# Performance work log

Hardware: AMD Instinct MI355X
Metric: run time of the kernel (lower is better)

## Reference

```python
import jax, jax.numpy as jnp
import numpy as np

ANCHORS = jnp.array([[1.3221, 1.73145], [3.19275, 4.00944], [5.05587, 8.09892],
                     [9.47112, 4.84053], [11.2364, 10.0071]], dtype=jnp.float32)
NUM_ANCHORS = 5
NUM_CLASSES = 20
MAX_BOXES = 50
NOOBJECT_SCALE = 1.0
OBJECT_SCALE = 5.0
COORD_SCALE = 1.0
CLASS_SCALE = 1.0
SIL_THRESH = 0.6


def iou_cwh(b1, b2):
    # boxes as (cx, cy, w, h); matches repo bbox_ious(x1y1x2y2=False)
    x1, y1, w1, h1 = b1[..., 0], b1[..., 1], b1[..., 2], b1[..., 3]
    x2, y2, w2, h2 = b2[..., 0], b2[..., 1], b2[..., 2], b2[..., 3]
    uw = jnp.maximum(x1 + w1 * 0.5, x2 + w2 * 0.5) - jnp.minimum(x1 - w1 * 0.5, x2 - w2 * 0.5)
    uh = jnp.maximum(y1 + h1 * 0.5, y2 + h2 * 0.5) - jnp.minimum(y1 - h1 * 0.5, y2 - h2 * 0.5)
    cw = w1 + w2 - uw
    ch = h1 + h2 - uh
    inter = jnp.where((cw <= 0) | (ch <= 0), 0.0, cw * ch)
    return inter / (w1 * h1 + w2 * h2 - inter)


def setup_inputs() -> dict:
    key = jax.random.key(0)
    k1, k2, k3, k4 = jax.random.split(key, 4)
    nB = 64
    output = jax.random.normal(k1, (nB, NUM_ANCHORS * (5 + NUM_CLASSES), 38, 38), dtype=jnp.float32)
    # target layout per box: (class, x, y, w, h), all normalized; x>0 marks a valid box
    cls_col = jax.random.randint(k2, (nB, MAX_BOXES, 1), 0, NUM_CLASSES).astype(jnp.float32)
    xy = jax.random.uniform(k3, (nB, MAX_BOXES, 2), minval=0.05, maxval=0.95)
    wh = jax.random.uniform(k4, (nB, MAX_BOXES, 2), minval=0.02, maxval=0.3)
    target = jnp.concatenate([cls_col, xy, wh], axis=-1).reshape(nB, MAX_BOXES * 5)
    return {"output": output, "target": target}


def region_loss(output, target):
    nB = output.shape[0]
    nA, nC = NUM_ANCHORS, NUM_CLASSES
    nH, nW = output.shape[2], output.shape[3]
    out = output.reshape(nB, nA, 5 + nC, nH, nW)
    x = jax.nn.sigmoid(out[:, :, 0])
    y = jax.nn.sigmoid(out[:, :, 1])
    w = out[:, :, 2]
    h = out[:, :, 3]
    conf = jax.nn.sigmoid(out[:, :, 4])
    # [nB,nA,nC,nH,nW] -> [nB*nA*nH*nW, nC] (matches torch transpose/view order)
    cls_logits = jnp.transpose(out[:, :, 5:], (0, 1, 3, 4, 2)).reshape(-1, nC)

    sg = jax.lax.stop_gradient
    aw, ah = ANCHORS[:, 0], ANCHORS[:, 1]
    grid_x = jnp.arange(nW, dtype=jnp.float32)[None, None, None, :]
    grid_y = jnp.arange(nH, dtype=jnp.float32)[None, None, :, None]
    px = sg(x) + grid_x
    py = sg(y) + grid_y
    pw = jnp.exp(sg(w)) * aw[None, :, None, None]
    ph = jnp.exp(sg(h)) * ah[None, :, None, None]
    pred_boxes = jnp.stack([px, py, pw, ph], axis=-1)  # [nB,nA,nH,nW,4]

    # ---- build_targets (vectorized) ----
    tgt = sg(target).reshape(nB, MAX_BOXES, 5)
    gcls = tgt[:, :, 0]
    gx = tgt[:, :, 1] * nW
    gy = tgt[:, :, 2] * nH
    gw = tgt[:, :, 3] * nW
    gh = tgt[:, :, 4] * nH
    # loop breaks at first x==0 -> cumulative validity
    valid = jnp.cumprod((tgt[:, :, 1] != 0).astype(jnp.int32), axis=1).astype(bool)

    # silence conf_mask where any-GT IoU > thresh
    pb_flat = pred_boxes.reshape(nB, nA * nH * nW, 4)
    gt_boxes = jnp.stack([gx, gy, gw, gh], axis=-1)  # [nB,50,4]
    ious = iou_cwh(pb_flat[:, :, None, :], gt_boxes[:, None, :, :])  # [nB,nAnc,50]
    ious = jnp.where(valid[:, None, :], ious, 0.0)
    max_iou = jnp.max(ious, axis=2)
    conf_mask = jnp.where(max_iou > SIL_THRESH, 0.0, NOOBJECT_SCALE).reshape(nB, nA, nH, nW)

    # seen < 12800 defaults
    shp = (nB, nA, nH, nW)
    coord_mask = jnp.ones(shp, jnp.float32)
    tx = jnp.full(shp, 0.5, jnp.float32)
    ty = jnp.full(shp, 0.5, jnp.float32)
    tw = jnp.zeros(shp, jnp.float32)
    th = jnp.zeros(shp, jnp.float32)
    tconf = jnp.zeros(shp, jnp.float32)
    tcls = jnp.zeros(shp, jnp.float32)
    cls_mask = jnp.zeros(shp, jnp.float32)

    # best anchor per GT by (0,0,w,h) IoU; argmax keeps first max like the strict '>' loop
    zA = jnp.zeros_like(aw)
    anchor_boxes = jnp.stack([zA, zA, aw, ah], axis=-1)  # [nA,4]
    zg = jnp.zeros_like(gw)
    gt_wh = jnp.stack([zg, zg, gw, gh], axis=-1)  # [nB,50,4]
    a_iou = iou_cwh(gt_wh[:, :, None, :], anchor_boxes[None, None, :, :])  # [nB,50,nA]
    best_n = jnp.argmax(a_iou, axis=2)  # [nB,50]

    gi = jnp.clip(gx.astype(jnp.int32), 0, nW - 1)
    gj = jnp.clip(gy.astype(jnp.int32), 0, nH - 1)
    aw_b = aw[best_n]
    ah_b = ah[best_n]
    tx_v = gx - gi.astype(jnp.float32)
    ty_v = gy - gj.astype(jnp.float32)
    tw_v = jnp.log(gw / aw_b)
    th_v = jnp.log(gh / ah_b)
    b_ix = jnp.arange(nB)
    pred_at = pred_boxes[b_ix[:, None], best_n, gj, gi]  # [nB,50,4]
    iou_gt = iou_cwh(gt_boxes, pred_at)  # [nB,50]

    def step(carry, t):
        cm, clm, tx_, ty_, tw_, th_, tcf, tcl = carry
        bsel = jnp.where(valid[:, t], b_ix, nB)  # out-of-bounds -> dropped
        n, j, i = best_n[:, t], gj[:, t], gi[:, t]
        st = lambda a, v: a.at[bsel, n, j, i].set(v, mode='drop')
        cm = st(cm, jnp.full((nB,), OBJECT_SCALE, jnp.float32))
        clm = st(clm, jnp.ones((nB,), jnp.float32))
        tx_ = st(tx_, tx_v[:, t])
        ty_ = st(ty_, ty_v[:, t])
        tw_ = st(tw_, tw_v[:, t])
        th_ = st(th_, th_v[:, t])
        tcf = st(tcf, iou_gt[:, t])
        tcl = st(tcl, gcls[:, t])
        return (cm, clm, tx_, ty_, tw_, th_, tcf, tcl), None

    init = (conf_mask, cls_mask, tx, ty, tw, th, tconf, tcls)
    (conf_mask, cls_mask, tx, ty, tw, th, tconf, tcls), _ = jax.lax.scan(
        step, init, jnp.arange(MAX_BOXES))

    # ---- losses ----
    cmf = jnp.sqrt(conf_mask)
    loss_x = COORD_SCALE * jnp.sum((x * coord_mask - tx * coord_mask) ** 2) / 2.0
    loss_y = COORD_SCALE * jnp.sum((y * coord_mask - ty * coord_mask) ** 2) / 2.0
    loss_w = COORD_SCALE * jnp.sum((w * coord_mask - tw * coord_mask) ** 2) / 2.0
    loss_h = COORD_SCALE * jnp.sum((h * coord_mask - th * coord_mask) ** 2) / 2.0
    loss_conf = jnp.sum((conf * cmf - tconf * cmf) ** 2) / 2.0
    logp = jax.nn.log_softmax(cls_logits, axis=-1)
    labels = tcls.reshape(-1).astype(jnp.int32)
    ce = -jnp.take_along_axis(logp, labels[:, None], axis=1)[:, 0]
    loss_cls = CLASS_SCALE * jnp.sum(ce * cls_mask.reshape(-1))
    return loss_x + loss_y + loss_w + loss_h + loss_conf + loss_cls


def reference(output, target):
    return region_loss(output, target)
```

## Files before the change

kernel.cpp:

```cpp
#include <hip/hip_runtime.h>
#include <math.h>

#define NA 5
#define NC 20
#define NH 38
#define NW 38
#define MAX_BOXES 50
#define SPAT (NH * NW)
#define CELLS_PER_B (NA * SPAT)
#define TPB 256
#define CELLS_PER_T 2
#define CPB (TPB * CELLS_PER_T)
#define GX ((CELLS_PER_B + CPB - 1) / CPB)
#define OBJECT_SCALE 5.0f
#define NOOBJECT_SCALE 1.0f

__constant__ float c_aw[NA]  = {1.3221f, 3.19275f, 5.05587f, 9.47112f, 11.2364f};
__constant__ float c_ah[NA]  = {1.73145f, 4.00944f, 8.09892f, 4.84053f, 10.0071f};
__constant__ float c_iaw[NA] = {1.f/1.3221f, 1.f/3.19275f, 1.f/5.05587f, 1.f/9.47112f, 1.f/11.2364f};
__constant__ float c_iah[NA] = {1.f/1.73145f, 1.f/4.00944f, 1.f/8.09892f, 1.f/4.84053f, 1.f/10.0071f};

__device__ __forceinline__ float fexp(float v) { return __expf(v); }
__device__ __forceinline__ float flog(float v) { return __logf(v); }
__device__ __forceinline__ float frcp(float v) { return __builtin_amdgcn_rcpf(v); }
__device__ __forceinline__ float fsig(float v) { return frcp(1.f + __expf(-v)); }

__device__ __forceinline__ float iou_fast(float x1, float y1, float w1, float h1,
                                          float x2, float y2, float w2, float h2) {
  float uw = fmaxf(x1 + w1 * 0.5f, x2 + w2 * 0.5f) - fminf(x1 - w1 * 0.5f, x2 - w2 * 0.5f);
  float uh = fmaxf(y1 + h1 * 0.5f, y2 + h2 * 0.5f) - fminf(y1 - h1 * 0.5f, y2 - h2 * 0.5f);
  float cw = w1 + w2 - uw;
  float ch = h1 + h2 - uh;
  float inter = (cw <= 0.f || ch <= 0.f) ? 0.f : cw * ch;
  return inter * frcp(w1 * h1 + w2 * h2 - inter);
}

__device__ __forceinline__ float iou_wh_exact(float w1, float h1, float w2, float h2) {
  float uw = fmaxf(w1 * 0.5f, w2 * 0.5f) - fminf(-w1 * 0.5f, -w2 * 0.5f);
  float uh = fmaxf(h1 * 0.5f, h2 * 0.5f) - fminf(-h1 * 0.5f, -h2 * 0.5f);
  float cw = w1 + w2 - uw;
  float ch = h1 + h2 - uh;
  float inter = (cw <= 0.f || ch <= 0.f) ? 0.f : cw * ch;
  return inter / (w1 * h1 + w2 * h2 - inter);
}

__global__ __launch_bounds__(64) void prep_kernel(
    const float* __restrict__ out, const float* __restrict__ target,
    float4* __restrict__ boxes, float* __restrict__ delta) {
  const int b = blockIdx.x;
  const int t = threadIdx.x;
  __shared__ float4 sb_lo[MAX_BOXES];
  __shared__ float  sb_ag[MAX_BOXES];

  float cls = 0.f, x = 0.f, y = 0.f, w = 0.f, h = 0.f;
  if (t < MAX_BOXES) {
    const float* tg = target + (size_t)(b * MAX_BOXES + t) * 5;
    cls = tg[0]; x = tg[1]; y = tg[2]; w = tg[3]; h = tg[4];
  }
  unsigned long long nz = __ballot(t < MAX_BOXES && x != 0.f);
  unsigned long long low = (t < 63) ? ((1ull << (t + 1)) - 1ull) : ~0ull;
  bool valid = (t < MAX_BOXES) && ((nz & low) == low);

  float gx = x * NW, gy = y * NH, gw = w * NW, gh = h * NH;

  int best = 0; float bestiou = -1.f;
#pragma unroll
  for (int a2 = 0; a2 < NA; ++a2) {
    float aiou = iou_wh_exact(gw, gh, c_aw[a2], c_ah[a2]);
    if (aiou > bestiou) { bestiou = aiou; best = a2; }
  }
  int gi = min(max((int)gx, 0), NW - 1);
  int gj = min(max((int)gy, 0), NH - 1);
  int cell = best * SPAT + gj * NW + gi;

  unsigned long long vm = __ballot(valid);
  bool winner = valid;
  for (int tp = 0; tp < MAX_BOXES; ++tp) {
    int c2 = __shfl(cell, tp);
    if (tp > t && ((vm >> tp) & 1ull) && c2 == cell) winner = false;
  }

  float4 lo; float ag;
  if (valid) {
    lo = make_float4(gx - gw * 0.5f, gx + gw * 0.5f, gy - gh * 0.5f, gy + gh * 0.5f);
    ag = 0.375f * (gw * gh);
  } else {
    lo = make_float4(1e30f, 1e30f, 1e30f, 1e30f);
    ag = 0.f;
  }
  if (t < MAX_BOXES) {
    boxes[(size_t)(b * MAX_BOXES + t) * 2]     = lo;
    boxes[(size_t)(b * MAX_BOXES + t) * 2 + 1] = make_float4(ag, 0.f, 0.f, 0.f);
    sb_lo[t] = lo;
    sb_ag[t] = ag;
  }
  __syncthreads();

  float d = 0.f;
  if (winner) {
    const float* bp = out + ((size_t)(b * NA + best) * 25) * SPAT + gj * NW + gi;
    float v0 = bp[0], v1 = bp[SPAT], v2 = bp[2 * SPAT], v3 = bp[3 * SPAT], v4 = bp[4 * SPAT];
    float xs = fsig(v0), ys = fsig(v1), cs = fsig(v4);
    float pw = fexp(v2) * c_aw[best], ph = fexp(v3) * c_ah[best];
    float px = xs + (float)gi, py = ys + (float)gj;
    float plx = px - pw * 0.5f, phx = px + pw * 0.5f;
    float ply = py - ph * 0.5f, phy = py + ph * 0.5f;
    float ap = 0.375f * (pw * ph);

    float msc = -1e30f;
    for (int t2 = 0; t2 < MAX_BOXES; ++t2) {
      float4 l2 = sb_lo[t2];
      float cw = fminf(phx, l2.y) - fmaxf(plx, l2.x);
      float ch = fminf(phy, l2.w) - fmaxf(ply, l2.z);
      cw = fmaxf(cw, 0.f);
      msc = fmaxf(msc, fmaf(cw, ch, -sb_ag[t2]));
    }
    float cmask_def = (msc > ap) ? 0.f : NOOBJECT_SCALE;
    float xd = xs - 0.5f, yd = ys - 0.5f;
    float D = 0.5f * (xd * xd + yd * yd + v2 * v2 + v3 * v3 + cmask_def * (cs * cs));

    float txv = gx - (float)gi, tyv = gy - (float)gj;
    float twv = flog(gw * c_iaw[best]), thv = flog(gh * c_iah[best]);
    float tconf = iou_fast(gx, gy, gw, gh, px, py, pw, ph);
    float dx = xs - txv, dy = ys - tyv, dwv = v2 - twv, dhv = v3 - thv, dc = cs - tconf;

    int label = (int)cls;
    const float* cb = bp + 5 * SPAT;
    float m = -1e30f, lv = 0.f;
    for (int c = 0; c < NC; ++c) {
      float vv = cb[c * SPAT];
      if (c == label) lv = vv;
      m = fmaxf(m, vv);
    }
    float ssum = 0.f;
    for (int c = 0; c < NC; ++c) ssum += fexp(cb[c * SPAT] - m);
    float ce = (m + flog(ssum)) - lv;

    float W = 0.5f * (dx * dx + dy * dy + dwv * dwv + dhv * dhv +
                      OBJECT_SCALE * (dc * dc)) + ce;
    d = W - D;
  }
  for (int o = 32; o > 0; o >>= 1) d += __shfl_down(d, o, 64);
  if (t == 0) delta[b] = d;
}

__global__ __launch_bounds__(TPB) void main_kernel(
    const float* __restrict__ out, const float4* __restrict__ boxes,
    float* __restrict__ partials) {
  const int b = blockIdx.y;
  const int s0 = blockIdx.x * CPB;
  const int tid = threadIdx.x;

  __shared__ float4 sb_lo[MAX_BOXES];
  __shared__ float  sb_ag[MAX_BOXES];
  __shared__ float  s_red[TPB / 64];

  if (tid < MAX_BOXES) {
    float4 lo = boxes[(size_t)(b * MAX_BOXES + tid) * 2];
    float4 hi = boxes[(size_t)(b * MAX_BOXES + tid) * 2 + 1];
    sb_lo[tid] = lo;
    sb_ag[tid] = hi.x;
  }
  __syncthreads();

  bool ok[CELLS_PER_T];
  float v0[CELLS_PER_T], v1[CELLS_PER_T], v2[CELLS_PER_T], v3[CELLS_PER_T], v4[CELLS_PER_T];
  float fi[CELLS_PER_T], fj[CELLS_PER_T], paw[CELLS_PER_T], pah[CELLS_PER_T];
#pragma unroll
  for (int q = 0; q < CELLS_PER_T; ++q) {
    int s = s0 + q * TPB + tid;
    ok[q] = (s < CELLS_PER_B);
    int sc = ok[q] ? s : 0;
    unsigned a = (unsigned)sc / SPAT;
    unsigned r = (unsigned)sc - a * SPAT;
    unsigned j = r / NW, i = r - j * NW;
    fi[q] = (float)i; fj[q] = (float)j;
    paw[q] = c_aw[a]; pah[q] = c_ah[a];
    const float* bp = out + ((size_t)(b * NA + a) * 25) * SPAT + r;
    v0[q] = bp[0];
    v1[q] = bp[SPAT];
    v2[q] = bp[2 * SPAT];
    v3[q] = bp[3 * SPAT];
    v4[q] = bp[4 * SPAT];
  }

  float xs[CELLS_PER_T], ys[CELLS_PER_T], cs[CELLS_PER_T];
  float plx[CELLS_PER_T], phx[CELLS_PER_T], ply[CELLS_PER_T], phy[CELLS_PER_T];
  float ap[CELLS_PER_T], msc[CELLS_PER_T];
#pragma unroll
  for (int q = 0; q < CELLS_PER_T; ++q) {
    xs[q] = fsig(v0[q]);
    ys[q] = fsig(v1[q]);
    cs[q] = fsig(v4[q]);
    float pw = fexp(v2[q]) * paw[q], ph = fexp(v3[q]) * pah[q];
    float px = xs[q] + fi[q], py = ys[q] + fj[q];
    plx[q] = px - pw * 0.5f; phx[q] = px + pw * 0.5f;
    ply[q] = py - ph * 0.5f; phy[q] = py + ph * 0.5f;
    ap[q] = 0.375f * (pw * ph);
    msc[q] = -1e30f;
  }

#pragma unroll
  for (int c0 = 0; c0 < MAX_BOXES; c0 += 10) {
    float4 bl[10]; float bag[10];
#pragma unroll
    for (int u = 0; u < 10; ++u) { bl[u] = sb_lo[c0 + u]; bag[u] = sb_ag[c0 + u]; }
#pragma unroll
    for (int u = 0; u < 10; ++u) {
#pragma unroll
      for (int q = 0; q < CELLS_PER_T; ++q) {
        float cw = fminf(phx[q], bl[u].y) - fmaxf(plx[q], bl[u].x);
        float ch = fminf(phy[q], bl[u].w) - fmaxf(ply[q], bl[u].z);
        cw = fmaxf(cw, 0.f);
        msc[q] = fmaxf(msc[q], fmaf(cw, ch, -bag[u]));
      }
    }
  }

  float acc = 0.f;
#pragma unroll
  for (int q = 0; q < CELLS_PER_T; ++q) {
    if (!ok[q]) continue;
    float cmask = (msc[q] > ap[q]) ? 0.f : NOOBJECT_SCALE;
    float xd = xs[q] - 0.5f, yd = ys[q] - 0.5f;
    acc += 0.5f * (xd * xd + yd * yd + v2[q] * v2[q] + v3[q] * v3[q] +
                   cmask * (cs[q] * cs[q]));
  }

  for (int o = 32; o > 0; o >>= 1) acc += __shfl_down(acc, o, 64);
  int wid = tid >> 6, lane = tid & 63;
  if (lane == 0) s_red[wid] = acc;
  __syncthreads();
  if (tid == 0) {
    float v = 0.f;
#pragma unroll
    for (int wdx = 0; wdx < TPB / 64; ++wdx) v += s_red[wdx];
    partials[blockIdx.y * GX + blockIdx.x] = v;
  }
}

__global__ __launch_bounds__(256) void reduce_kernel(
    const float* __restrict__ vals, int n, float* __restrict__ outv) {
  float acc = 0.f;
  for (int i = threadIdx.x; i < n; i += 256) acc += vals[i];
  for (int o = 32; o > 0; o >>= 1) acc += __shfl_down(acc, o, 64);
  __shared__ float s_red[4];
  int wid = threadIdx.x >> 6, lane = threadIdx.x & 63;
  if (lane == 0) s_red[wid] = acc;
  __syncthreads();
  if (threadIdx.x == 0) outv[0] = s_red[0] + s_red[1] + s_red[2] + s_red[3];
}

extern "C" void kernel_launch(void* const* d_in, const int* in_sizes, int n_in,
                              void* d_out, int out_size, void* d_ws, size_t ws_size,
                              hipStream_t stream) {
  const float* out = (const float*)d_in[0];
  const float* target = (const float*)d_in[1];
  int nB = in_sizes[0] / (NA * (5 + NC) * SPAT);

  float4* boxes = (float4*)d_ws;
  float* partials = (float*)((char*)d_ws + (size_t)nB * MAX_BOXES * 2 * sizeof(float4));
  float* delta = partials + GX * nB;

  hipLaunchKernelGGL(prep_kernel, dim3(nB), dim3(64), 0, stream,
                     out, target, boxes, delta);
  hipLaunchKernelGGL(main_kernel, dim3(GX, nB), dim3(TPB), 0, stream,
                     out, boxes, partials);
  hipLaunchKernelGGL(reduce_kernel, dim3(1), dim3(256), 0, stream,
                     partials, GX * nB + nB, (float*)d_out);
}
```

Before: 107.0 us.

## Fuse prep kernel into main kernel with per-block box recomputation

Removes the separate prep kernel. Every main block now rebuilds the per-image box table from the target array in shared memory, and one extra block per image computes the responsible-cell correction term. This drops a kernel launch and the global round trip of the box table, at the cost of redundant target loads and box math in every block. The class-logit loads for the correction term are also hoisted into a register array so they are read once.

```diff
diff --git a/kernel.cpp b/kernel.cpp
--- a/kernel.cpp
+++ b/kernel.cpp
@@ -12,6 +12,7 @@
 #define CELLS_PER_T 2
 #define CPB (TPB * CELLS_PER_T)
 #define GX ((CELLS_PER_B + CPB - 1) / CPB)
+#define GXP (GX + 1)
 #define OBJECT_SCALE 5.0f
 #define NOOBJECT_SCALE 1.0f
 
@@ -44,124 +45,114 @@
   return inter / (w1 * h1 + w2 * h2 - inter);
 }
 
-__global__ __launch_bounds__(64) void prep_kernel(
+__global__ __launch_bounds__(TPB) void fused_kernel(
     const float* __restrict__ out, const float* __restrict__ target,
-    float4* __restrict__ boxes, float* __restrict__ delta) {
-  const int b = blockIdx.x;
-  const int t = threadIdx.x;
-  __shared__ float4 sb_lo[MAX_BOXES];
-  __shared__ float  sb_ag[MAX_BOXES];
-
-  float cls = 0.f, x = 0.f, y = 0.f, w = 0.f, h = 0.f;
-  if (t < MAX_BOXES) {
-    const float* tg = target + (size_t)(b * MAX_BOXES + t) * 5;
-    cls = tg[0]; x = tg[1]; y = tg[2]; w = tg[3]; h = tg[4];
-  }
-  unsigned long long nz = __ballot(t < MAX_BOXES && x != 0.f);
-  unsigned long long low = (t < 63) ? ((1ull << (t + 1)) - 1ull) : ~0ull;
-  bool valid = (t < MAX_BOXES) && ((nz & low) == low);
-
-  float gx = x * NW, gy = y * NH, gw = w * NW, gh = h * NH;
-
-  int best = 0; float bestiou = -1.f;
-#pragma unroll
-  for (int a2 = 0; a2 < NA; ++a2) {
-    float aiou = iou_wh_exact(gw, gh, c_aw[a2], c_ah[a2]);
-    if (aiou > bestiou) { bestiou = aiou; best = a2; }
-  }
-  int gi = min(max((int)gx, 0), NW - 1);
-  int gj = min(max((int)gy, 0), NH - 1);
-  int cell = best * SPAT + gj * NW + gi;
-
-  unsigned long long vm = __ballot(valid);
-  bool winner = valid;
-  for (int tp = 0; tp < MAX_BOXES; ++tp) {
-    int c2 = __shfl(cell, tp);
-    if (tp > t && ((vm >> tp) & 1ull) && c2 == cell) winner = false;
-  }
-
-  float4 lo; float ag;
-  if (valid) {
-    lo = make_float4(gx - gw * 0.5f, gx + gw * 0.5f, gy - gh * 0.5f, gy + gh * 0.5f);
-    ag = 0.375f * (gw * gh);
-  } else {
-    lo = make_float4(1e30f, 1e30f, 1e30f, 1e30f);
-    ag = 0.f;
-  }
-  if (t < MAX_BOXES) {
-    boxes[(size_t)(b * MAX_BOXES + t) * 2]     = lo;
-    boxes[(size_t)(b * MAX_BOXES + t) * 2 + 1] = make_float4(ag, 0.f, 0.f, 0.f);
-    sb_lo[t] = lo;
-    sb_ag[t] = ag;
-  }
-  __syncthreads();
-
-  float d = 0.f;
-  if (winner) {
-    const float* bp = out + ((size_t)(b * NA + best) * 25) * SPAT + gj * NW + gi;
-    float v0 = bp[0], v1 = bp[SPAT], v2 = bp[2 * SPAT], v3 = bp[3 * SPAT], v4 = bp[4 * SPAT];
-    float xs = fsig(v0), ys = fsig(v1), cs = fsig(v4);
-    float pw = fexp(v2) * c_aw[best], ph = fexp(v3) * c_ah[best];
-    float px = xs + (float)gi, py = ys + (float)gj;
-    float plx = px - pw * 0.5f, phx = px + pw * 0.5f;
-    float ply = py - ph * 0.5f, phy = py + ph * 0.5f;
-    float ap = 0.375f * (pw * ph);
-
-    float msc = -1e30f;
-    for (int t2 = 0; t2 < MAX_BOXES; ++t2) {
-      float4 l2 = sb_lo[t2];
-      float cw = fminf(phx, l2.y) - fmaxf(plx, l2.x);
-      float ch = fminf(phy, l2.w) - fmaxf(ply, l2.z);
-      cw = fmaxf(cw, 0.f);
-      msc = fmaxf(msc, fmaf(cw, ch, -sb_ag[t2]));
-    }
-    float cmask_def = (msc > ap) ? 0.f : NOOBJECT_SCALE;
-    float xd = xs - 0.5f, yd = ys - 0.5f;
-    float D = 0.5f * (xd * xd + yd * yd + v2 * v2 + v3 * v3 + cmask_def * (cs * cs));
-
-    float txv = gx - (float)gi, tyv = gy - (float)gj;
-    float twv = flog(gw * c_iaw[best]), thv = flog(gh * c_iah[best]);
-    float tconf = iou_fast(gx, gy, gw, gh, px, py, pw, ph);
-    float dx = xs - txv, dy = ys - tyv, dwv = v2 - twv, dhv = v3 - thv, dc = cs - tconf;
-
-    int label = (int)cls;
-    const float* cb = bp + 5 * SPAT;
-    float m = -1e30f, lv = 0.f;
-    for (int c = 0; c < NC; ++c) {
-      float vv = cb[c * SPAT];
-      if (c == label) lv = vv;
-      m = fmaxf(m, vv);
-    }
-    float ssum = 0.f;
-    for (int c = 0; c < NC; ++c) ssum += fexp(cb[c * SPAT] - m);
-    float ce = (m + flog(ssum)) - lv;
-
-    float W = 0.5f * (dx * dx + dy * dy + dwv * dwv + dhv * dhv +
-                      OBJECT_SCALE * (dc * dc)) + ce;
-    d = W - D;
-  }
-  for (int o = 32; o > 0; o >>= 1) d += __shfl_down(d, o, 64);
-  if (t == 0) delta[b] = d;
-}
-
-__global__ __launch_bounds__(TPB) void main_kernel(
-    const float* __restrict__ out, const float4* __restrict__ boxes,
     float* __restrict__ partials) {
   const int b = blockIdx.y;
-  const int s0 = blockIdx.x * CPB;
   const int tid = threadIdx.x;
 
   __shared__ float4 sb_lo[MAX_BOXES];
   __shared__ float  sb_ag[MAX_BOXES];
   __shared__ float  s_red[TPB / 64];
 
-  if (tid < MAX_BOXES) {
-    float4 lo = boxes[(size_t)(b * MAX_BOXES + tid) * 2];
-    float4 hi = boxes[(size_t)(b * MAX_BOXES + tid) * 2 + 1];
-    sb_lo[tid] = lo;
-    sb_ag[tid] = hi.x;
-  }
-  __syncthreads();
+  if (blockIdx.x == GX) {
+    const int t = tid;
+    const bool w0 = (tid < 64);
+    float cls = 0.f, x = 0.f, y = 0.f, w = 0.f, h = 0.f;
+    float gx = 0.f, gy = 0.f, gw = 0.f, gh = 0.f;
+    bool winner = false;
+    int best = 0, gi = 0, gj = 0;
+    if (w0) {
+      if (t < MAX_BOXES) {
+        const float* tg = target + (size_t)(b * MAX_BOXES + t) * 5;
+        cls = tg[0]; x = tg[1]; y = tg[2]; w = tg[3]; h = tg[4];
+      }
+      unsigned long long nz = __ballot(t < MAX_BOXES && x != 0.f);
+      unsigned long long low = (t < 63) ? ((1ull << (t + 1)) - 1ull) : ~0ull;
+      bool valid = (t < MAX_BOXES) && ((nz & low) == low);
+      gx = x * NW; gy = y * NH; gw = w * NW; gh = h * NH;
+
+      float bestiou = -1.f;
+#pragma unroll
+      for (int a2 = 0; a2 < NA; ++a2) {
+        float aiou = iou_wh_exact(gw, gh, c_aw[a2], c_ah[a2]);
+        if (aiou > bestiou) { bestiou = aiou; best = a2; }
+      }
+      gi = min(max((int)gx, 0), NW - 1);
+      gj = min(max((int)gy, 0), NH - 1);
+      int cell = best * SPAT + gj * NW + gi;
+
+      unsigned long long vm = __ballot(valid);
+      winner = valid;
+      for (int tp = 0; tp < MAX_BOXES; ++tp) {
+        int c2 = __shfl(cell, tp);
+        if (tp > t && ((vm >> tp) & 1ull) && c2 == cell) winner = false;
+      }
+      if (t < MAX_BOXES) {
+        if (valid) {
+          sb_lo[t] = make_float4(gx - gw * 0.5f, gx + gw * 0.5f, gy - gh * 0.5f, gy + gh * 0.5f);
+          sb_ag[t] = 0.375f * (gw * gh);
+        } else {
+          sb_lo[t] = make_float4(1e30f, 1e30f, 1e30f, 1e30f);
+          sb_ag[t] = 0.f;
+        }
+      }
+    }
+    __syncthreads();
+
+    float d = 0.f;
+    if (w0 && winner) {
+      const float* bp = out + ((size_t)(b * NA + best) * 25) * SPAT + gj * NW + gi;
+      float v0 = bp[0], v1 = bp[SPAT], v2 = bp[2 * SPAT], v3 = bp[3 * SPAT], v4 = bp[4 * SPAT];
+      float xs = fsig(v0), ys = fsig(v1), cs = fsig(v4);
+      float pw = fexp(v2) * c_aw[best], ph = fexp(v3) * c_ah[best];
+      float px = xs + (float)gi, py = ys + (float)gj;
+      float plx = px - pw * 0.5f, phx = px + pw * 0.5f;
+      float ply = py - ph * 0.5f, phy = py + ph * 0.5f;
+      float ap = 0.375f * (pw * ph);
+
+      float msc = -1e30f;
+      for (int t2 = 0; t2 < MAX_BOXES; ++t2) {
+        float4 l2 = sb_lo[t2];
+        float cw = fminf(phx, l2.y) - fmaxf(plx, l2.x);
+        float ch = fminf(phy, l2.w) - fmaxf(ply, l2.z);
+        cw = fmaxf(cw, 0.f);
+        msc = fmaxf(msc, fmaf(cw, ch, -sb_ag[t2]));
+      }
+      float cmask_def = (msc > ap) ? 0.f : NOOBJECT_SCALE;
+      float xd = xs - 0.5f, yd = ys - 0.5f;
+      float D = 0.5f * (xd * xd + yd * yd + v2 * v2 + v3 * v3 + cmask_def * (cs * cs));
+
+      float txv = gx - (float)gi, tyv = gy - (float)gj;
+      float twv = flog(gw * c_iaw[best]), thv = flog(gh * c_iah[best]);
+      float tconf = iou_fast(gx, gy, gw, gh, px, py, pw, ph);
+      float dx = xs - txv, dy = ys - tyv, dwv = v2 - twv, dhv = v3 - thv, dc = cs - tconf;
+
+      int label = (int)cls;
+      const float* cb = bp + 5 * SPAT;
+      float vv[NC];
+#pragma unroll
+      for (int c = 0; c < NC; ++c) vv[c] = cb[c * SPAT];
+      float m = -1e30f, lv = 0.f;
+#pragma unroll
+      for (int c = 0; c < NC; ++c) { if (c == label) lv = vv[c]; m = fmaxf(m, vv[c]); }
+      float ssum = 0.f;
+#pragma unroll
+      for (int c = 0; c < NC; ++c) ssum += fexp(vv[c] - m);
+      float ce = (m + flog(ssum)) - lv;
+
+      float W = 0.5f * (dx * dx + dy * dy + dwv * dwv + dhv * dhv +
+                        OBJECT_SCALE * (dc * dc)) + ce;
+      d = W - D;
+    }
+    if (w0) {
+      for (int o = 32; o > 0; o >>= 1) d += __shfl_down(d, o, 64);
+      if (tid == 0) partials[(size_t)b * GXP + GX] = d;
+    }
+    return;
+  }
+
+  const int s0 = blockIdx.x * CPB;
 
   bool ok[CELLS_PER_T];
   float v0[CELLS_PER_T], v1[CELLS_PER_T], v2[CELLS_PER_T], v3[CELLS_PER_T], v4[CELLS_PER_T];
@@ -184,6 +175,28 @@
     v4[q] = bp[4 * SPAT];
   }
 
+  if (tid < 64) {
+    const int t = tid;
+    float x = 0.f, y = 0.f, w = 0.f, h = 0.f;
+    if (t < MAX_BOXES) {
+      const float* tg = target + (size_t)(b * MAX_BOXES + t) * 5;
+      x = tg[1]; y = tg[2]; w = tg[3]; h = tg[4];
+    }
+    unsigned long long nz = __ballot(t < MAX_BOXES && x != 0.f);
+    unsigned long long low = (t < 63) ? ((1ull << (t + 1)) - 1ull) : ~0ull;
+    bool valid = (t < MAX_BOXES) && ((nz & low) == low);
+    float gx = x * NW, gy = y * NH, gw = w * NW, gh = h * NH;
+    if (t < MAX_BOXES) {
+      if (valid) {
+        sb_lo[t] = make_float4(gx - gw * 0.5f, gx + gw * 0.5f, gy - gh * 0.5f, gy + gh * 0.5f);
+        sb_ag[t] = 0.375f * (gw * gh);
+      } else {
+        sb_lo[t] = make_float4(1e30f, 1e30f, 1e30f, 1e30f);
+        sb_ag[t] = 0.f;
+      }
+    }
+  }
+
   float xs[CELLS_PER_T], ys[CELLS_PER_T], cs[CELLS_PER_T];
   float plx[CELLS_PER_T], phx[CELLS_PER_T], ply[CELLS_PER_T], phy[CELLS_PER_T];
   float ap[CELLS_PER_T], msc[CELLS_PER_T];
@@ -199,6 +212,7 @@
     ap[q] = 0.375f * (pw * ph);
     msc[q] = -1e30f;
   }
+  __syncthreads();
 
 #pragma unroll
   for (int c0 = 0; c0 < MAX_BOXES; c0 += 10) {
@@ -235,7 +249,7 @@
     float v = 0.f;
 #pragma unroll
     for (int wdx = 0; wdx < TPB / 64; ++wdx) v += s_red[wdx];
-    partials[blockIdx.y * GX + blockIdx.x] = v;
+    partials[(size_t)b * GXP + blockIdx.x] = v;
   }
 }
 
@@ -258,14 +272,10 @@
   const float* target = (const float*)d_in[1];
   int nB = in_sizes[0] / (NA * (5 + NC) * SPAT);
 
-  float4* boxes = (float4*)d_ws;
-  float* partials = (float*)((char*)d_ws + (size_t)nB * MAX_BOXES * 2 * sizeof(float4));
-  float* delta = partials + GX * nB;
-
-  hipLaunchKernelGGL(prep_kernel, dim3(nB), dim3(64), 0, stream,
-                     out, target, boxes, delta);
-  hipLaunchKernelGGL(main_kernel, dim3(GX, nB), dim3(TPB), 0, stream,
-                     out, boxes, partials);
+  float* partials = (float*)d_ws;
+
+  hipLaunchKernelGGL(fused_kernel, dim3(GXP, nB), dim3(TPB), 0, stream,
+                     out, target, partials);
   hipLaunchKernelGGL(reduce_kernel, dim3(1), dim3(256), 0, stream,
-                     partials, GX * nB + nB, (float*)d_out);
-}
+                     partials, GXP * nB, (float*)d_out);
+}
```

Result: slower. 116.7 us (+9.0%).
